# Performance work log

Hardware: AMD Instinct MI355X
Metric: run time of the kernel (lower is better)

The kernel has to match this reference:

```python
import jax, jax.numpy as jnp
import numpy as np

V, E, HID, T, B, S = 50000, 256, 512, 9, 64, 512
H = HID // 2
START, STOP = T - 2, T - 1
NEG = -100000.0


def setup_inputs() -> dict:
    key = jax.random.key(0)
    ks = jax.random.split(key, 16)
    sc = 0.05
    tr = jax.random.normal(ks[15], (T, T), jnp.float32)
    tr = tr.at[STOP, :].set(NEG).at[:, START].set(NEG)
    return {
        "batchSentence": jax.random.randint(ks[0], (B, S), 0, V),
        "batchTag": jax.random.randint(ks[1], (B, S), 0, T - 2),
        "lenList": jax.random.randint(ks[2], (B,), 1, S + 1),
        "emb": jax.random.normal(ks[3], (V, E), jnp.float32) * sc,
        "w_ih0": jax.random.normal(ks[4], (2, 4 * H, E), jnp.float32) * sc,
        "w_hh0": jax.random.normal(ks[5], (2, 4 * H, H), jnp.float32) * sc,
        "b_ih0": jax.random.normal(ks[6], (2, 4 * H), jnp.float32) * sc,
        "b_hh0": jax.random.normal(ks[7], (2, 4 * H), jnp.float32) * sc,
        "w_ih1": jax.random.normal(ks[8], (2, 4 * H, 2 * H), jnp.float32) * sc,
        "w_hh1": jax.random.normal(ks[9], (2, 4 * H, H), jnp.float32) * sc,
        "b_ih1": jax.random.normal(ks[10], (2, 4 * H), jnp.float32) * sc,
        "b_hh1": jax.random.normal(ks[11], (2, 4 * H), jnp.float32) * sc,
        "fc_w": jax.random.normal(ks[12], (T, HID), jnp.float32) * sc,
        "fc_b": jax.random.normal(ks[13], (T,), jnp.float32) * sc,
        "transitions": tr,
    }


def _lstm_dir(xs, w_ih, w_hh, b_ih, b_hh, reverse):
    # xs: [S, B, in]; PyTorch gate order i, f, g, o
    h0 = jnp.zeros((xs.shape[1], w_hh.shape[1]), xs.dtype)
    b = b_ih + b_hh

    def step(carry, x_t):
        h, c = carry
        g = x_t @ w_ih.T + h @ w_hh.T + b
        i, f, gg, o = jnp.split(g, 4, axis=-1)
        c = jax.nn.sigmoid(f) * c + jax.nn.sigmoid(i) * jnp.tanh(gg)
        h = jax.nn.sigmoid(o) * jnp.tanh(c)
        return (h, c), h

    _, hs = jax.lax.scan(step, (h0, h0), xs, reverse=reverse)
    return hs


def _bilstm(x, layers):
    xs = x.transpose(1, 0, 2)  # [S, B, E]
    for w_ih, w_hh, b_ih, b_hh in layers:
        fwd = _lstm_dir(xs, w_ih[0], w_hh[0], b_ih[0], b_hh[0], False)
        bwd = _lstm_dir(xs, w_ih[1], w_hh[1], b_ih[1], b_hh[1], True)
        xs = jnp.concatenate([fwd, bwd], axis=-1)
    return xs.transpose(1, 0, 2)  # [B, S, 2H]


def _crf_forward(feats, mask, trans):
    # feats: [B, S, T], mask: [B, S] (t < length)
    start = jnp.full((feats.shape[0], feats.shape[2]), NEG, feats.dtype).at[:, START].set(0.0)

    def step(alpha, inp):
        ft, mt = inp  # [B, T], [B]
        new = jax.nn.logsumexp(alpha[:, :, None] + trans[None, :, :], axis=1) + ft
        return jnp.where(mt[:, None], new, alpha), None

    alpha, _ = jax.lax.scan(step, start, (feats.transpose(1, 0, 2), mask.T))
    return jax.nn.logsumexp(alpha + trans[None, :, STOP], axis=1)


def _gold_score(feats, tags, lengths, trans):
    # Faithful to original _score_sentence, incl. the feats[i][tags[i+1]] indexing
    Ss = feats.shape[1]
    pos = jnp.arange(Ss)
    pair_valid = (pos[None, :-1] + 1) < lengths[:, None]  # step i -> i+1 exists
    em0 = jnp.take_along_axis(feats[:, 0, :], tags[:, :1], axis=1)[:, 0]
    em_shift = jnp.take_along_axis(feats[:, :-1, :], tags[:, 1:, None], axis=2)[:, :, 0]
    tr = trans[tags[:, :-1], tags[:, 1:]]
    body = jnp.sum(jnp.where(pair_valid, tr + em_shift, 0.0), axis=1)
    last_tag = jnp.take_along_axis(tags, (lengths - 1)[:, None], axis=1)[:, 0]
    return trans[START, tags[:, 0]] + em0 + body + trans[last_tag, STOP]


def reference(batchSentence, batchTag, lenList, emb, w_ih0, w_hh0, b_ih0, b_hh0,
              w_ih1, w_hh1, b_ih1, b_hh1, fc_w, fc_b, transitions):
    x = emb[batchSentence]  # [B, S, E]
    h = _bilstm(x, [(w_ih0, w_hh0, b_ih0, b_hh0), (w_ih1, w_hh1, b_ih1, b_hh1)])
    feats = h @ fc_w.T + fc_b  # [B, S, T]
    mask = jnp.arange(feats.shape[1])[None, :] < lenList[:, None]
    forward_score = _crf_forward(feats, mask, transitions)
    gold_score = _gold_score(feats, batchTag, lenList, transitions)
    return jnp.mean(forward_score - gold_score)
```

## Files before the change

### kernel.cpp

```cpp
#include <hip/hip_runtime.h>
#include <math.h>

#define NEGV (-100000.0f)
constexpr int Bn = 64, Sn = 512, En = 256, Hn = 256, HIDn = 512, Tn = 9;
constexpr int START_T = Tn - 2, STOP_T = Tn - 1;
constexpr int Mn = Bn * Sn;

typedef unsigned int u32;
typedef unsigned short u16;
typedef unsigned long long u64;
typedef short short8 __attribute__((ext_vector_type(8)));
typedef float f32x4 __attribute__((ext_vector_type(4)));
typedef int i32x4 __attribute__((ext_vector_type(4)));

__device__ __forceinline__ float sigf(float x) { return 1.0f / (1.0f + __expf(-x)); }
__device__ __forceinline__ float tanh_f(float x) { return 2.0f / (1.0f + __expf(-2.0f * x)) - 1.0f; }
__device__ __forceinline__ u16 f2bf(float f) {
  u32 u = __float_as_uint(f);
  return (u16)((u + 0x7fffu + ((u >> 16) & 1u)) >> 16);
}
__device__ __forceinline__ float bflo(u32 u) { return __uint_as_float(u << 16); }
__device__ __forceinline__ float bfhi(u32 u) { return __uint_as_float(u & 0xffff0000u); }
__device__ __forceinline__ float b2f(u16 v) { return __uint_as_float((u32)v << 16); }

__device__ __forceinline__ void bar_lds() {
  __builtin_amdgcn_sched_barrier(0);
  asm volatile("s_waitcnt lgkmcnt(0)" ::: "memory");
  __builtin_amdgcn_s_barrier();
  __builtin_amdgcn_sched_barrier(0);
}

__global__ void prep_scales(const float* __restrict__ whh0, const float* __restrict__ whh1,
                            float* __restrict__ sw0, float* __restrict__ dqs0,
                            float* __restrict__ sw1, float* __restrict__ dqs1) {
  int r = blockIdx.x * blockDim.x + threadIdx.x;
  if (r >= 2048) return;
  const float* p0 = whh0 + (size_t)r * 256;
  const float* p1 = whh1 + (size_t)r * 256;
  float m0 = 0.f, m1 = 0.f;
  for (int k = 0; k < 256; ++k) {
    m0 = fmaxf(m0, fabsf(p0[k]));
    m1 = fmaxf(m1, fabsf(p1[k]));
  }
  m0 = fmaxf(m0, 1e-8f); m1 = fmaxf(m1, 1e-8f);
  sw0[r] = m0 / 127.f; dqs0[r] = m0 / (127.f * 127.f);
  sw1[r] = m1 / 127.f; dqs1[r] = m1 / (127.f * 127.f);
}

__global__ void prep_kernel(const float* __restrict__ wih0, const float* __restrict__ whh0,
                            const float* __restrict__ bih0, const float* __restrict__ bhh0,
                            const float* __restrict__ wih1, const float* __restrict__ whh1,
                            const float* __restrict__ bih1, const float* __restrict__ bhh1,
                            const float* __restrict__ fcw,
                            u16* __restrict__ wifrag0, u16* __restrict__ wifrag1,
                            char* __restrict__ wq0, char* __restrict__ wq1,
                            const float* __restrict__ sw0, const float* __restrict__ sw1,
                            float* __restrict__ bias0, float* __restrict__ bias1,
                            u16* __restrict__ fcfrag) {
  int tid = blockIdx.x * blockDim.x + threadIdx.x;
  int nth = gridDim.x * blockDim.x;
  for (int idx = tid; idx < 524288; idx += nth) {
    int j = idx & 7, lane = (idx >> 3) & 63, ks = (idx >> 9) & 7,
        w2 = (idx >> 12) & 3, nb = (idx >> 14) & 15, d = (idx >> 18) & 1;
    int n = nb * 64 + w2 * 16 + (lane & 15);
    int k = ks * 32 + ((lane >> 4) & 3) * 8 + j;
    wifrag0[idx] = f2bf(wih0[(d * 1024 + n) * 256 + k]);
  }
  for (int idx = tid; idx < 1048576; idx += nth) {
    int j = idx & 7, lane = (idx >> 3) & 63, ks = (idx >> 9) & 15,
        w2 = (idx >> 13) & 3, nb = (idx >> 15) & 15, d = (idx >> 19) & 1;
    int n = nb * 64 + w2 * 16 + (lane & 15);
    int k = ks * 32 + ((lane >> 4) & 3) * 8 + j;
    wifrag1[idx] = f2bf(wih1[(d * 1024 + n) * 512 + k]);
  }
  for (int idx = tid; idx < 524288; idx += nth) {
    int j = idx & 15, lane = (idx >> 4) & 63, kt = (idx >> 10) & 3,
        q = (idx >> 12) & 7, wv = (idx >> 15) & 7, d = (idx >> 18) & 1;
    int nt = q * 8 + wv;
    int n = nt * 16 + (lane & 15);
    int k = kt * 64 + ((lane >> 4) & 3) * 16 + j;
    int row = d * 1024 + n;
    float v0 = whh0[(size_t)row * 256 + k] / sw0[row];
    float v1 = whh1[(size_t)row * 256 + k] / sw1[row];
    wq0[idx] = (char)(int)fminf(fmaxf(rintf(v0), -127.f), 127.f);
    wq1[idx] = (char)(int)fminf(fmaxf(rintf(v1), -127.f), 127.f);
  }
  for (int idx = tid; idx < 8192; idx += nth) {
    int j = idx & 7, lane = (idx >> 3) & 63, ks = (idx >> 9) & 15;
    int tag = lane & 15;
    int k = ks * 32 + ((lane >> 4) & 3) * 8 + j;
    fcfrag[idx] = (tag < Tn) ? f2bf(fcw[(size_t)tag * HIDn + k]) : (u16)0;
  }
  for (int idx = tid; idx < 2 * 1024; idx += nth) {
    bias0[idx] = bih0[idx] + bhh0[idx];
    bias1[idx] = bih1[idx] + bhh1[idx];
  }
}

template <int KS, bool GATHER>
__global__ __launch_bounds__(256) void gemm_ih(
    const void* __restrict__ xsrc_v,
    const int* __restrict__ sent,
    const uint4* __restrict__ wifrag,
    const float* __restrict__ bias,
    u16* __restrict__ gx2)
{
  constexpr int K = KS * 32;
  constexpr int PITCH = K + 8;
  __shared__ u16 As[64][PITCH];
  const int tid = threadIdx.x;
  const int l = tid & 63;
  const int w = tid >> 6;
  const int col = l & 15;
  const int quad = (l >> 4) & 3;
  const int m0 = blockIdx.x * 64;
  const int dir = blockIdx.y;

  {
    const int lr = tid >> 2, lq = tid & 3;
    if constexpr (GATHER) {
      const float4* xrow = reinterpret_cast<const float4*>(
          (const float*)xsrc_v + (size_t)sent[m0 + lr] * 256) + lq * 16;
      u32* dst = reinterpret_cast<u32*>(&As[lr][lq * 64]);
#pragma unroll
      for (int i = 0; i < 16; ++i) {
        float4 v = xrow[i];
        dst[i * 2 + 0] = (u32)f2bf(v.x) | ((u32)f2bf(v.y) << 16);
        dst[i * 2 + 1] = (u32)f2bf(v.z) | ((u32)f2bf(v.w) << 16);
      }
    } else {
      const uint4* xrow = reinterpret_cast<const uint4*>(
          (const u16*)xsrc_v + (size_t)(m0 + lr) * 512) + lq * 16;
      uint4* dst = reinterpret_cast<uint4*>(&As[lr][lq * 128]);
#pragma unroll
      for (int i = 0; i < 16; ++i) dst[i] = xrow[i];
    }
  }
  __syncthreads();

  const uint4* wfd = wifrag + (size_t)dir * 16 * 4 * KS * 64;
#pragma unroll 1
  for (int nb = 0; nb < 16; ++nb) {
    uint4 bf[KS];
#pragma unroll
    for (int ks = 0; ks < KS; ++ks)
      bf[ks] = wfd[((nb * 4 + w) * KS + ks) * 64 + l];

    f32x4 acc[4];
#pragma unroll
    for (int mt = 0; mt < 4; ++mt) acc[mt] = (f32x4){0.f, 0.f, 0.f, 0.f};
#pragma unroll
    for (int ks = 0; ks < KS; ++ks) {
      short8 b8 = __builtin_bit_cast(short8, bf[ks]);
#pragma unroll
      for (int mt = 0; mt < 4; ++mt) {
        uint4 av = *reinterpret_cast<const uint4*>(&As[mt * 16 + col][ks * 32 + quad * 8]);
        acc[mt] = __builtin_amdgcn_mfma_f32_16x16x32_bf16(
            __builtin_bit_cast(short8, av), b8, acc[mt], 0, 0, 0);
      }
    }

    const int n = nb * 64 + w * 16 + col;
    const int gate = n >> 8, unit = n & 255;
    const float bv = bias[dir * 1024 + n];
#pragma unroll
    for (int mt = 0; mt < 4; ++mt) {
#pragma unroll
      for (int r = 0; r < 4; ++r) {
        int m = m0 + mt * 16 + quad * 4 + r;
        gx2[((size_t)(dir * Mn + m) * 256 + unit) * 4 + gate] = f2bf(acc[mt][r] + bv);
      }
    }
  }
}

__global__ __launch_bounds__(512, 2) void lstm_recur_v13(
    const i32x4* __restrict__ wq,
    const float* __restrict__ dqs,
    const u16* __restrict__ gx2,
    u16* __restrict__ out)
{
  __shared__ char Ah8[2][2][288];
  __shared__ int accW[8][2][32][4];
  const int tid = threadIdx.x;
  const int l = tid & 63;
  const int w = tid >> 6;
  const int col = l & 15;
  const int quad = (l >> 4) & 3;
  const int dir = blockIdx.x >> 5;
  const int bq = blockIdx.x & 31;

  i32x4 bw[8][4];
  {
    const i32x4* wp = wq + ((size_t)dir * 8 + w) * 8 * 4 * 64;
#pragma unroll
    for (int q = 0; q < 8; ++q)
#pragma unroll
      for (int kt = 0; kt < 4; ++kt)
        bw[q][kt] = wp[(q * 4 + kt) * 64 + l];
  }

  const int r_ep = l >> 5;
  const int ue = l & 31;
  const int e_ep = ue >> 4, c_ep = ue & 15;
  const int unit = e_ep * 128 + w * 16 + c_ep;

  float sc[4];
#pragma unroll
  for (int g = 0; g < 4; ++g)
    sc[g] = dqs[dir * 1024 + g * 256 + unit];

  const int mrow = bq * 2 + r_ep;
  const uint2* gp = reinterpret_cast<const uint2*>(gx2) +
                    (size_t)(dir * Mn + mrow * Sn) * 256 + unit;
  u16* op = out + (size_t)mrow * Sn * HIDn + dir * Hn + unit;

  float c_st = 0.f;

  for (int s = 0; s < Sn; ++s) {
    const int t = dir ? (Sn - 1 - s) : s;
    uint2 g2 = gp[(size_t)t * 256];

    auto epi = [&](float a0, float a1, float a2, float a3) {
      float gi_ = a0 + b2f((u16)(g2.x & 0xffff));
      float gf_ = a1 + b2f((u16)(g2.x >> 16));
      float gg_ = a2 + b2f((u16)(g2.y & 0xffff));
      float go_ = a3 + b2f((u16)(g2.y >> 16));
      c_st = sigf(gf_) * c_st + sigf(gi_) * tanh_f(gg_);
      float h = sigf(go_) * tanh_f(c_st);
      Ah8[s & 1][r_ep][unit] = (char)(int)rintf(h * 127.f);
      op[(size_t)t * HIDn] = f2bf(h);
    };

    if (s > 0) {
      const int rb = (s + 1) & 1;
      i32x4 av[4];
#pragma unroll
      for (int kt = 0; kt < 4; ++kt)
        av[kt] = *reinterpret_cast<const i32x4*>(
            &Ah8[rb][col & 1][kt * 64 + quad * 16]);

      i32x4 acc[8];
#pragma unroll
      for (int q = 0; q < 8; ++q) acc[q] = (i32x4){0, 0, 0, 0};

#pragma unroll
      for (int kt = 0; kt < 4; ++kt)
#pragma unroll
        for (int g = 0; g < 4; ++g)
          acc[g * 2] = __builtin_amdgcn_mfma_i32_16x16x64_i8(av[kt], bw[g * 2][kt], acc[g * 2], 0, 0, 0);
      if (quad == 0) {
#pragma unroll
        for (int r = 0; r < 2; ++r) {
          i32x4 v = (i32x4){acc[0][r], acc[2][r], acc[4][r], acc[6][r]};
          *reinterpret_cast<i32x4*>(&accW[w][r][col][0]) = v;
        }
      }
      i32x4 qA = *reinterpret_cast<const i32x4*>(&accW[w][r_ep][ue][0]);

#pragma unroll
      for (int kt = 0; kt < 4; ++kt)
#pragma unroll
        for (int g = 0; g < 4; ++g)
          acc[g * 2 + 1] = __builtin_amdgcn_mfma_i32_16x16x64_i8(av[kt], bw[g * 2 + 1][kt], acc[g * 2 + 1], 0, 0, 0);

      if (ue < 16)
        epi((float)qA[0] * sc[0], (float)qA[1] * sc[1],
            (float)qA[2] * sc[2], (float)qA[3] * sc[3]);

      if (quad == 0) {
#pragma unroll
        for (int r = 0; r < 2; ++r) {
          i32x4 v = (i32x4){acc[1][r], acc[3][r], acc[5][r], acc[7][r]};
          *reinterpret_cast<i32x4*>(&accW[w][r][16 + col][0]) = v;
        }
      }
      i32x4 qB = *reinterpret_cast<const i32x4*>(&accW[w][r_ep][ue][0]);
      if (ue >= 16)
        epi((float)qB[0] * sc[0], (float)qB[1] * sc[1],
            (float)qB[2] * sc[2], (float)qB[3] * sc[3]);
    } else {
      epi(0.f, 0.f, 0.f, 0.f);
    }
    bar_lds();
  }
}

__global__ __launch_bounds__(256) void fc_mfma(const u16* __restrict__ out1,
                                               const uint4* __restrict__ fcfrag,
                                               const float* __restrict__ fcb,
                                               float* __restrict__ feats) {
  __shared__ u16 As[64][520];
  const int tid = threadIdx.x;
  const int l = tid & 63;
  const int w = tid >> 6;
  const int col = l & 15;
  const int quad = (l >> 4) & 3;
  const int m0 = blockIdx.x * 64;

  {
    const int lr = tid >> 2, lq = tid & 3;
    const uint4* xrow = reinterpret_cast<const uint4*>(
        out1 + (size_t)(m0 + lr) * 512) + lq * 16;
    uint4* dst = reinterpret_cast<uint4*>(&As[lr][lq * 128]);
#pragma unroll
    for (int i = 0; i < 16; ++i) dst[i] = xrow[i];
  }
  __syncthreads();

  uint4 bf[16];
#pragma unroll
  for (int ks = 0; ks < 16; ++ks) bf[ks] = fcfrag[ks * 64 + l];

  f32x4 acc = (f32x4){0.f, 0.f, 0.f, 0.f};
#pragma unroll
  for (int ks = 0; ks < 16; ++ks) {
    uint4 av = *reinterpret_cast<const uint4*>(&As[w * 16 + col][ks * 32 + quad * 8]);
    acc = __builtin_amdgcn_mfma_f32_16x16x32_bf16(
        __builtin_bit_cast(short8, av), __builtin_bit_cast(short8, bf[ks]), acc, 0, 0, 0);
  }

  if (col < Tn) {
    const float bv = fcb[col];
#pragma unroll
    for (int r = 0; r < 4; ++r) {
      int m = m0 + w * 16 + quad * 4 + r;
      feats[(size_t)m * Tn + col] = acc[r] + bv;
    }
  }
}

__global__ __launch_bounds__(64) void crf_kernel(const float* __restrict__ feats,
                                                 const int* __restrict__ tags,
                                                 const int* __restrict__ lens,
                                                 const float* __restrict__ trans,
                                                 float* __restrict__ scores) {
  const int b = blockIdx.x;
  const int j = threadIdx.x;
  const int jj = j < Tn ? j : Tn - 1;
  const int len = lens[b];

  float trc[Tn];
#pragma unroll
  for (int i = 0; i < Tn; ++i) trc[i] = trans[i * Tn + jj];
  const float trS = trans[jj * Tn + STOP_T];

  float alpha = (j == START_T) ? 0.0f : NEGV;
  const float* fb = feats + (size_t)b * Sn * Tn;

  for (int t = 0; t < Sn; ++t) {
    float f = (j < Tn) ? fb[t * Tn + j] : 0.0f;
    float v[Tn];
    float m = -3.0e38f;
#pragma unroll
    for (int i = 0; i < Tn; ++i) {
      float ai = __shfl(alpha, i);
      v[i] = ai + trc[i];
      m = fmaxf(m, v[i]);
    }
    float ssum = 0.0f;
#pragma unroll
    for (int i = 0; i < Tn; ++i) ssum += __expf(v[i] - m);
    float newa = m + __logf(ssum) + f;
    if (t < len && j < Tn) alpha = newa;
  }

  float val = (j < Tn) ? alpha + trS : -3.0e38f;
  float m = val;
#pragma unroll
  for (int off = 32; off; off >>= 1) m = fmaxf(m, __shfl_xor(m, off));
  float se = (j < Tn) ? __expf(val - m) : 0.0f;
#pragma unroll
  for (int off = 32; off; off >>= 1) se += __shfl_xor(se, off);
  float fscore = m + __logf(se);

  const int* tg = tags + b * Sn;
  float part = 0.0f;
  for (int q = 0; q < 8; ++q) {
    int s0 = j * 8 + q;
    if (s0 < Sn - 1 && (s0 + 1) < len) {
      int ta = tg[s0], tb = tg[s0 + 1];
      part += trans[ta * Tn + tb] + fb[s0 * Tn + tb];
    }
  }
#pragma unroll
  for (int off = 32; off; off >>= 1) part += __shfl_xor(part, off);

  if (j == 0) {
    int t0 = tg[0];
    int tl = tg[len - 1];
    float gold = trans[START_T * Tn + t0] + fb[0 * Tn + t0] + part + trans[tl * Tn + STOP_T];
    scores[b] = fscore - gold;
  }
}

__global__ void finalize_kernel(const float* __restrict__ scores, float* __restrict__ out) {
  int l = threadIdx.x;
  float v = scores[l];
#pragma unroll
  for (int off = 32; off; off >>= 1) v += __shfl_xor(v, off);
  if (l == 0) out[0] = v / 64.0f;
}

extern "C" void kernel_launch(void* const* d_in, const int* in_sizes, int n_in,
                              void* d_out, int out_size, void* d_ws, size_t ws_size,
                              hipStream_t stream) {
  const int* sent = (const int*)d_in[0];
  const int* tags = (const int*)d_in[1];
  const int* lens = (const int*)d_in[2];
  const float* emb = (const float*)d_in[3];
  const float* wih0 = (const float*)d_in[4];
  const float* whh0 = (const float*)d_in[5];
  const float* bih0 = (const float*)d_in[6];
  const float* bhh0 = (const float*)d_in[7];
  const float* wih1 = (const float*)d_in[8];
  const float* whh1 = (const float*)d_in[9];
  const float* bih1 = (const float*)d_in[10];
  const float* bhh1 = (const float*)d_in[11];
  const float* fcw = (const float*)d_in[12];
  const float* fcb = (const float*)d_in[13];
  const float* trans = (const float*)d_in[14];

  char* ws = (char*)d_ws;
  u16* outb = (u16*)ws;
  u16* gx2 = (u16*)(ws + 33554432);
  float* feats = (float*)gx2;
  char* p = ws + 33554432 + 134217728;
  float* scores = (float*)p;            p += 256;
  float* bias0 = (float*)p;             p += 8192;
  float* bias1 = (float*)p;             p += 8192;
  u16* wifrag0 = (u16*)p;               p += 1048576;
  u16* wifrag1 = (u16*)p;               p += 2097152;
  char* wq0 = p;                        p += 524288;
  char* wq1 = p;                        p += 524288;
  float* sw0 = (float*)p;               p += 8192;
  float* dqs0 = (float*)p;              p += 8192;
  float* sw1 = (float*)p;               p += 8192;
  float* dqs1 = (float*)p;              p += 8192;
  u16* fcfrag = (u16*)p;                p += 16384;

  prep_scales<<<8, 256, 0, stream>>>(whh0, whh1, sw0, dqs0, sw1, dqs1);
  prep_kernel<<<2048, 256, 0, stream>>>(wih0, whh0, bih0, bhh0, wih1, whh1, bih1, bhh1, fcw,
                                        wifrag0, wifrag1, wq0, wq1, sw0, sw1, bias0, bias1,
                                        fcfrag);

  dim3 ggrid(Mn / 64, 2);
  gemm_ih<8, true><<<ggrid, 256, 0, stream>>>(emb, sent, (const uint4*)wifrag0, bias0, gx2);
  lstm_recur_v13<<<64, 512, 0, stream>>>((const i32x4*)wq0, dqs0, gx2, outb);
  gemm_ih<16, false><<<ggrid, 256, 0, stream>>>(outb, nullptr, (const uint4*)wifrag1, bias1, gx2);
  lstm_recur_v13<<<64, 512, 0, stream>>>((const i32x4*)wq1, dqs1, gx2, outb);

  fc_mfma<<<Mn / 64, 256, 0, stream>>>(outb, (const uint4*)fcfrag, fcb, feats);
  crf_kernel<<<Bn, 64, 0, stream>>>(feats, tags, lens, trans, scores);
  finalize_kernel<<<1, 64, 0, stream>>>(scores, (float*)d_out);
}
```

Before: 2.070 ms.

## Interleave two batch groups per LSTM recurrence block to overlap MFMA and epilogue

Each recurrent block now handles four batch rows, split into two independent groups A and B, instead of two, which halves the grid to 32 blocks. The step loop is software-pipelined so that group B's gate epilogue from the previous step runs while group A's MFMAs are in flight, and the reverse. The aim is to hide the serial epilogue latency (sigmoid, tanh, LDS exchange) behind matrix work in the latency-bound recurrence. In exchange it uses half as many CUs, two barriers per step, and more LDS, and it leaves a redundant duplicated line in the B init.

Result: slower. 2.647 ms (+27.9%).

```diff
diff --git a/kernel.cpp b/kernel.cpp
--- a/kernel.cpp
+++ b/kernel.cpp
@@ -174,21 +174,23 @@
   }
 }
 
-__global__ __launch_bounds__(512, 2) void lstm_recur_v13(
+__global__ __launch_bounds__(512, 2) void lstm_recur_v14(
     const i32x4* __restrict__ wq,
     const float* __restrict__ dqs,
     const u16* __restrict__ gx2,
     u16* __restrict__ out)
 {
-  __shared__ char Ah8[2][2][288];
-  __shared__ int accW[8][2][32][4];
+  __shared__ char AhA[2][2][288];
+  __shared__ char AhB[2][2][288];
+  __shared__ int accWA[8][2][32][4];
+  __shared__ int accWB[8][2][32][4];
   const int tid = threadIdx.x;
   const int l = tid & 63;
   const int w = tid >> 6;
   const int col = l & 15;
   const int quad = (l >> 4) & 3;
-  const int dir = blockIdx.x >> 5;
-  const int bq = blockIdx.x & 31;
+  const int dir = blockIdx.x >> 4;
+  const int bq = blockIdx.x & 15;
 
   i32x4 bw[8][4];
   {
@@ -210,79 +212,139 @@
   for (int g = 0; g < 4; ++g)
     sc[g] = dqs[dir * 1024 + g * 256 + unit];
 
-  const int mrow = bq * 2 + r_ep;
-  const uint2* gp = reinterpret_cast<const uint2*>(gx2) +
-                    (size_t)(dir * Mn + mrow * Sn) * 256 + unit;
-  u16* op = out + (size_t)mrow * Sn * HIDn + dir * Hn + unit;
-
-  float c_st = 0.f;
-
-  for (int s = 0; s < Sn; ++s) {
-    const int t = dir ? (Sn - 1 - s) : s;
-    uint2 g2 = gp[(size_t)t * 256];
-
-    auto epi = [&](float a0, float a1, float a2, float a3) {
-      float gi_ = a0 + b2f((u16)(g2.x & 0xffff));
-      float gf_ = a1 + b2f((u16)(g2.x >> 16));
-      float gg_ = a2 + b2f((u16)(g2.y & 0xffff));
-      float go_ = a3 + b2f((u16)(g2.y >> 16));
-      c_st = sigf(gf_) * c_st + sigf(gi_) * tanh_f(gg_);
-      float h = sigf(go_) * tanh_f(c_st);
-      Ah8[s & 1][r_ep][unit] = (char)(int)rintf(h * 127.f);
-      op[(size_t)t * HIDn] = f2bf(h);
-    };
-
-    if (s > 0) {
-      const int rb = (s + 1) & 1;
+  const int mrowA = bq * 4 + r_ep;
+  const int mrowB = bq * 4 + 2 + r_ep;
+  const uint2* gpA = reinterpret_cast<const uint2*>(gx2) +
+                     (size_t)(dir * Mn + mrowA * Sn) * 256 + unit;
+  const uint2* gpB = reinterpret_cast<const uint2*>(gx2) +
+                     (size_t)(dir * Mn + mrowB * Sn) * 256 + unit;
+  u16* opA = out + (size_t)mrowA * Sn * HIDn + dir * Hn + unit;
+  u16* opB = out + (size_t)mrowB * Sn * HIDn + dir * Hn + unit;
+
+  float cA = 0.f, cB = 0.f;
+
+  {
+    const int t0 = dir ? (Sn - 1) : 0;
+    uint2 gA0 = gpA[(size_t)t0 * 256];
+    uint2 gB0 = gpB[(size_t)t0 * 256];
+    {
+      float gi_ = b2f((u16)(gA0.x & 0xffff));
+      float gg_ = b2f((u16)(gA0.y & 0xffff));
+      float go_ = b2f((u16)(gA0.y >> 16));
+      cA = sigf(gi_) * tanh_f(gg_);
+      float h = sigf(go_) * tanh_f(cA);
+      AhA[0][r_ep][unit] = (char)(int)rintf(h * 127.f);
+      opA[(size_t)t0 * HIDn] = f2bf(h);
+    }
+    {
+      float gi_ = b2f((u16)(gB0.x & 0xffff));
+      float gg_ = b2f((u16)(gB0.y & 0xffff));
+      float go_ = b2f((u16)(gB0.y >> 16));
+      cB = sigf(gi_) * tanh_f(gB0.y & 0xffff ? b2f((u16)(gB0.y & 0xffff)) : 0.f);
+      cB = sigf(gi_) * tanh_f(b2f((u16)(gB0.y & 0xffff)));
+      float h = sigf(go_) * tanh_f(cB);
+      AhB[0][r_ep][unit] = (char)(int)rintf(h * 127.f);
+      opB[(size_t)t0 * HIDn] = f2bf(h);
+    }
+    bar_lds();
+  }
+
+  uint2 gB_prev = (uint2){0u, 0u};
+  int t_prev = 0;
+
+  for (int i = 1; i < Sn; ++i) {
+    const int t = dir ? (Sn - 1 - i) : i;
+    const int rb = (i + 1) & 1, wb = i & 1;
+    uint2 gA_cur = gpA[(size_t)t * 256];
+    uint2 gB_cur = gpB[(size_t)t * 256];
+
+    {
       i32x4 av[4];
 #pragma unroll
       for (int kt = 0; kt < 4; ++kt)
-        av[kt] = *reinterpret_cast<const i32x4*>(
-            &Ah8[rb][col & 1][kt * 64 + quad * 16]);
-
+        av[kt] = *reinterpret_cast<const i32x4*>(&AhA[rb][col & 1][kt * 64 + quad * 16]);
       i32x4 acc[8];
 #pragma unroll
       for (int q = 0; q < 8; ++q) acc[q] = (i32x4){0, 0, 0, 0};
-
 #pragma unroll
       for (int kt = 0; kt < 4; ++kt)
 #pragma unroll
-        for (int g = 0; g < 4; ++g)
-          acc[g * 2] = __builtin_amdgcn_mfma_i32_16x16x64_i8(av[kt], bw[g * 2][kt], acc[g * 2], 0, 0, 0);
+        for (int q = 0; q < 8; ++q)
+          acc[q] = __builtin_amdgcn_mfma_i32_16x16x64_i8(av[kt], bw[q][kt], acc[q], 0, 0, 0);
       if (quad == 0) {
 #pragma unroll
-        for (int r = 0; r < 2; ++r) {
-          i32x4 v = (i32x4){acc[0][r], acc[2][r], acc[4][r], acc[6][r]};
-          *reinterpret_cast<i32x4*>(&accW[w][r][col][0]) = v;
-        }
+        for (int e = 0; e < 2; ++e)
+#pragma unroll
+          for (int r = 0; r < 2; ++r) {
+            i32x4 v = (i32x4){acc[0 + e][r], acc[2 + e][r], acc[4 + e][r], acc[6 + e][r]};
+            *reinterpret_cast<i32x4*>(&accWA[w][r][e * 16 + col][0]) = v;
+          }
       }
-      i32x4 qA = *reinterpret_cast<const i32x4*>(&accW[w][r_ep][ue][0]);
-
+    }
+
+    if (i > 1) {
+      i32x4 q0 = *reinterpret_cast<const i32x4*>(&accWB[w][r_ep][ue][0]);
+      float gi_ = fmaf((float)q0[0], sc[0], b2f((u16)(gB_prev.x & 0xffff)));
+      float gf_ = fmaf((float)q0[1], sc[1], b2f((u16)(gB_prev.x >> 16)));
+      float gg_ = fmaf((float)q0[2], sc[2], b2f((u16)(gB_prev.y & 0xffff)));
+      float go_ = fmaf((float)q0[3], sc[3], b2f((u16)(gB_prev.y >> 16)));
+      cB = sigf(gf_) * cB + sigf(gi_) * tanh_f(gg_);
+      float h = sigf(go_) * tanh_f(cB);
+      AhB[(i - 1) & 1][r_ep][unit] = (char)(int)rintf(h * 127.f);
+      opB[(size_t)t_prev * HIDn] = f2bf(h);
+    }
+    bar_lds();
+
+    {
+      i32x4 av[4];
 #pragma unroll
       for (int kt = 0; kt < 4; ++kt)
-#pragma unroll
-        for (int g = 0; g < 4; ++g)
-          acc[g * 2 + 1] = __builtin_amdgcn_mfma_i32_16x16x64_i8(av[kt], bw[g * 2 + 1][kt], acc[g * 2 + 1], 0, 0, 0);
-
-      if (ue < 16)
-        epi((float)qA[0] * sc[0], (float)qA[1] * sc[1],
-            (float)qA[2] * sc[2], (float)qA[3] * sc[3]);
-
+        av[kt] = *reinterpret_cast<const i32x4*>(&AhB[rb][col & 1][kt * 64 + quad * 16]);
+      i32x4 acc[8];
+#pragma unroll
+      for (int q = 0; q < 8; ++q) acc[q] = (i32x4){0, 0, 0, 0};
+#pragma unroll
+      for (int kt = 0; kt < 4; ++kt)
+#pragma unroll
+        for (int q = 0; q < 8; ++q)
+          acc[q] = __builtin_amdgcn_mfma_i32_16x16x64_i8(av[kt], bw[q][kt], acc[q], 0, 0, 0);
       if (quad == 0) {
 #pragma unroll
-        for (int r = 0; r < 2; ++r) {
-          i32x4 v = (i32x4){acc[1][r], acc[3][r], acc[5][r], acc[7][r]};
-          *reinterpret_cast<i32x4*>(&accW[w][r][16 + col][0]) = v;
-        }
+        for (int e = 0; e < 2; ++e)
+#pragma unroll
+          for (int r = 0; r < 2; ++r) {
+            i32x4 v = (i32x4){acc[0 + e][r], acc[2 + e][r], acc[4 + e][r], acc[6 + e][r]};
+            *reinterpret_cast<i32x4*>(&accWB[w][r][e * 16 + col][0]) = v;
+          }
       }
-      i32x4 qB = *reinterpret_cast<const i32x4*>(&accW[w][r_ep][ue][0]);
-      if (ue >= 16)
-        epi((float)qB[0] * sc[0], (float)qB[1] * sc[1],
-            (float)qB[2] * sc[2], (float)qB[3] * sc[3]);
-    } else {
-      epi(0.f, 0.f, 0.f, 0.f);
+    }
+
+    {
+      i32x4 q0 = *reinterpret_cast<const i32x4*>(&accWA[w][r_ep][ue][0]);
+      float gi_ = fmaf((float)q0[0], sc[0], b2f((u16)(gA_cur.x & 0xffff)));
+      float gf_ = fmaf((float)q0[1], sc[1], b2f((u16)(gA_cur.x >> 16)));
+      float gg_ = fmaf((float)q0[2], sc[2], b2f((u16)(gA_cur.y & 0xffff)));
+      float go_ = fmaf((float)q0[3], sc[3], b2f((u16)(gA_cur.y >> 16)));
+      cA = sigf(gf_) * cA + sigf(gi_) * tanh_f(gg_);
+      float h = sigf(go_) * tanh_f(cA);
+      AhA[wb][r_ep][unit] = (char)(int)rintf(h * 127.f);
+      opA[(size_t)t * HIDn] = f2bf(h);
     }
     bar_lds();
+
+    gB_prev = gB_cur;
+    t_prev = t;
+  }
+
+  {
+    i32x4 q0 = *reinterpret_cast<const i32x4*>(&accWB[w][r_ep][ue][0]);
+    float gi_ = fmaf((float)q0[0], sc[0], b2f((u16)(gB_prev.x & 0xffff)));
+    float gf_ = fmaf((float)q0[1], sc[1], b2f((u16)(gB_prev.x >> 16)));
+    float gg_ = fmaf((float)q0[2], sc[2], b2f((u16)(gB_prev.y & 0xffff)));
+    float go_ = fmaf((float)q0[3], sc[3], b2f((u16)(gB_prev.y >> 16)));
+    cB = sigf(gf_) * cB + sigf(gi_) * tanh_f(gg_);
+    float h = sigf(go_) * tanh_f(cB);
+    opB[(size_t)t_prev * HIDn] = f2bf(h);
   }
 }
 
@@ -446,9 +508,9 @@
 
   dim3 ggrid(Mn / 64, 2);
   gemm_ih<8, true><<<ggrid, 256, 0, stream>>>(emb, sent, (const uint4*)wifrag0, bias0, gx2);
-  lstm_recur_v13<<<64, 512, 0, stream>>>((const i32x4*)wq0, dqs0, gx2, outb);
+  lstm_recur_v14<<<32, 512, 0, stream>>>((const i32x4*)wq0, dqs0, gx2, outb);
   gemm_ih<16, false><<<ggrid, 256, 0, stream>>>(outb, nullptr, (const uint4*)wifrag1, bias1, gx2);
-  lstm_recur_v13<<<64, 512, 0, stream>>>((const i32x4*)wq1, dqs1, gx2, outb);
+  lstm_recur_v14<<<32, 512, 0, stream>>>((const i32x4*)wq1, dqs1, gx2, outb);
 
   fc_mfma<<<Mn / 64, 256, 0, stream>>>(outb, (const uint4*)fcfrag, fcb, feats);
   crf_kernel<<<Bn, 64, 0, stream>>>(feats, tags, lens, trans, scores);
```
